# Kernel tuning notes

Measured on AMD Instinct MI355X. Metric: run time of the kernel, lower is better.

The kernel has to match this reference:

```python
import jax, jax.numpy as jnp
import numpy as np

B, L, TOPK, NUM_RBF, NUM_POS, MAX_REL, CH = 4, 1024, 30, 16, 16, 32, 128
EDGE_IN = NUM_POS + NUM_RBF * 25 + 18  # 434
NODE_IN = 22


def _normalize(x, axis=-1):
    n = jnp.linalg.norm(x, axis=axis, keepdims=True)
    return jnp.where(n > 0, x / jnp.where(n > 0, n, 1.0), 0.0)


def layer_norm(x, g, b, eps=1e-5):
    mu = jnp.mean(x, axis=-1, keepdims=True)
    var = jnp.var(x, axis=-1, keepdims=True)
    return (x - mu) / jnp.sqrt(var + eps) * g + b


def gather_nodes_d(nodes, idx):
    # nodes [B,M,C], idx [B,N,K] -> [B,N,K,C]
    Bn, N, K = idx.shape
    out = jnp.take_along_axis(nodes, idx.reshape(Bn, N * K, 1), axis=1)
    return out.reshape(Bn, N, K, nodes.shape[-1])


def gather_edges(edges, idx):
    # edges [B,N,N,C], idx [B,N,K] -> [B,N,K,C]
    return jnp.take_along_axis(edges, idx[..., None], axis=2)


def cal_dihedral(Xf, eps=1e-7):
    U = _normalize(Xf[:, 1:, :] - Xf[:, :-1, :])
    u_0, u_1, u_2 = U[:, :-2], U[:, 1:-1], U[:, 2:]
    n_0 = _normalize(jnp.cross(u_0, u_1))
    n_1 = _normalize(jnp.cross(u_1, u_2))
    cosD = jnp.clip(jnp.sum(n_0 * n_1, -1), -1 + eps, 1 - eps)
    v = _normalize(jnp.cross(n_0, n_1))
    return jnp.sign(jnp.sum(-v * u_1, -1)) * jnp.arccos(cosD)


def _dihedrals(X, eps=1e-7):
    Bn, N = X.shape[0], X.shape[1]
    Xf = X[:, :, :3, :].reshape(Bn, 3 * N, 3)
    D = jnp.pad(cal_dihedral(Xf), ((0, 0), (1, 2))).reshape(Bn, N, 3)
    dihedral_feats = jnp.concatenate([jnp.cos(D), jnp.sin(D)], -1)
    U = _normalize(Xf[:, 1:, :] - Xf[:, :-1, :])
    cosA = jnp.clip(jnp.sum(U[:, :-2] * U[:, 1:-1], -1), -1 + eps, 1 - eps)
    A = jnp.pad(jnp.arccos(cosA), ((0, 0), (1, 2))).reshape(Bn, N, 3)
    angle_feats = jnp.concatenate([jnp.cos(A), jnp.sin(A)], -1)
    return jnp.concatenate([dihedral_feats, angle_feats], -1)  # [B,N,12]


def _quaternions(R):
    diag = jnp.diagonal(R, axis1=-2, axis2=-1)
    Rxx, Ryy, Rzz = diag[..., 0], diag[..., 1], diag[..., 2]
    mags = 0.5 * jnp.sqrt(jnp.abs(1.0 + jnp.stack([Rxx - Ryy - Rzz, -Rxx + Ryy - Rzz, -Rxx - Ryy + Rzz], -1)))
    signs = jnp.sign(jnp.stack([R[..., 2, 1] - R[..., 1, 2], R[..., 0, 2] - R[..., 2, 0], R[..., 1, 0] - R[..., 0, 1]], -1))
    w = jnp.sqrt(jax.nn.relu(1.0 + jnp.sum(diag, -1, keepdims=True))) / 2.0
    return _normalize(jnp.concatenate([signs * mags, w], -1))


def _orientations_coarse_gl_tuple(X, E_idx):
    V = X  # [B,N,4,3]
    Bn, N = X.shape[0], X.shape[1]
    Xf = X[:, :, :3, :].reshape(Bn, 3 * N, 3)
    U = _normalize(Xf[:, 1:, :] - Xf[:, :-1, :])
    u_0, u_1 = U[:, :-2], U[:, 1:-1]
    n_0 = _normalize(jnp.cross(u_0, u_1))[:, ::3]  # [B,N-1,3]
    b_1 = _normalize(u_0 - u_1)[:, ::3]
    Xa = Xf[:, ::3]  # N-atom coords [B,N,3]
    Q = jnp.stack([b_1, n_0, jnp.cross(b_1, n_0)], 2).reshape(Bn, N - 1, 9)
    Q = jnp.pad(Q, ((0, 0), (0, 1), (0, 0)))  # [B,N,9]
    Qm = Q.reshape(Bn, N, 3, 3)
    Q_neighbors = gather_nodes_d(Q, E_idx).reshape(Bn, N, -1, 3, 3)
    X_nb = gather_nodes_d(V[:, :, 1, :], E_idx)
    N_nb = gather_nodes_d(V[:, :, 0, :], E_idx)
    C_nb = gather_nodes_d(V[:, :, 2, :], E_idx)
    O_nb = gather_nodes_d(V[:, :, 3, :], E_idx)
    dXn = jnp.stack([X_nb, N_nb, C_nb, O_nb], 3) - Xa[:, :, None, None, :]  # [B,N,K,4,3]
    dU = jnp.einsum('bnij,bnkaj->bnkai', Qm, dXn)
    Kn = E_idx.shape[-1]
    E_direct = _normalize(dU).reshape(Bn, N, Kn, 12)
    R = jnp.einsum('bnji,bnkjl->bnkil', Qm, Q_neighbors)
    q = _quaternions(R)  # [B,N,K,4]
    dX_inner = V[:, :, jnp.array([0, 2, 3]), :] - Xa[:, :, None, :]
    V_direct = _normalize(jnp.einsum('bnij,bnaj->bnai', Qm, dX_inner)).reshape(Bn, N, 9)
    return V_direct, E_direct, q


def _dist(Xc, mask, eps=1e-6):
    mask_2D = mask[:, None, :] * mask[:, :, None]
    D = mask_2D * jnp.sqrt(jnp.sum((Xc[:, None, :, :] - Xc[:, :, None, :]) ** 2, -1) + eps)
    D_max = jnp.max(D, -1, keepdims=True)
    D_adjust = D + (1.0 - mask_2D) * D_max
    negD, E_idx = jax.lax.top_k(-D_adjust, min(TOPK, Xc.shape[1]))
    return -negD, E_idx


def _dist_seq(res_idx):
    D = jnp.abs(res_idx[:, :, None] - res_idx[:, None, :])
    _, E_idx = jax.lax.top_k(-D, min(TOPK, res_idx.shape[1]))
    return E_idx


def _rbf(D):
    D_mu = jnp.linspace(2.0, 22.0, NUM_RBF)
    D_sigma = (22.0 - 2.0) / NUM_RBF
    return jnp.exp(-(((D[..., None] - D_mu) / D_sigma) ** 2))


def _get_rbf(A, Bm, E_idx):
    D = jnp.sqrt(jnp.sum((A[:, :, None, :] - Bm[:, None, :, :]) ** 2, -1) + 1e-6)
    return _rbf(gather_edges(D[..., None], E_idx)[..., 0])


PAIRS = [('N', 'N'), ('C', 'C'), ('O', 'O'), ('Cb', 'Cb'), ('Ca', 'N'), ('Ca', 'C'), ('Ca', 'O'), ('Ca', 'Cb'),
         ('N', 'C'), ('N', 'O'), ('N', 'Cb'), ('Cb', 'C'), ('Cb', 'O'), ('O', 'C'), ('N', 'Ca'), ('C', 'Ca'),
         ('O', 'Ca'), ('Cb', 'Ca'), ('C', 'N'), ('O', 'N'), ('Cb', 'N'), ('C', 'Cb'), ('O', 'Cb'), ('C', 'O')]


def _forward(X, mask, residue_idx, chain_labels, W_pos, b_pos, W_edge, W_node, g_edge, b_edge, g_node, b_node):
    bvec = X[:, :, 1, :] - X[:, :, 0, :]
    cvec = X[:, :, 2, :] - X[:, :, 1, :]
    avec = jnp.cross(bvec, cvec)
    Cb = -0.58273431 * avec + 0.56802827 * bvec - 0.54067466 * cvec + X[:, :, 1, :]
    atoms = {'N': X[:, :, 0, :], 'Ca': X[:, :, 1, :], 'C': X[:, :, 2, :], 'O': X[:, :, 3, :], 'Cb': Cb}
    D_neighbors, E_idx = _dist(atoms['Ca'], mask)
    E_idx_res = _dist_seq(residue_idx)
    E_idx = jnp.where(mask[:, :, None] == 0, E_idx_res, E_idx)
    RBF_all = [_rbf(D_neighbors)]
    for pa, pb in PAIRS:
        RBF_all.append(_get_rbf(atoms[pa], atoms[pb], E_idx))
    RBF_all = jnp.concatenate(RBF_all, -1)  # [B,L,K,400]
    V_angles = _dihedrals(X) * mask[..., None]
    V_direct, E_direct, E_angles = _orientations_coarse_gl_tuple(X, E_idx)
    V_direct = V_direct * mask[..., None]
    offset = residue_idx[:, :, None] - residue_idx[:, None, :]
    E_offset = gather_edges(offset[..., None], E_idx)[..., 0]
    d_chains = (chain_labels[:, :, None] == chain_labels[:, None, :]).astype(jnp.int32)
    E_chains = gather_edges(d_chains[..., None], E_idx)[..., 0]
    d = jnp.clip(E_offset + MAX_REL, 0, 2 * MAX_REL) * E_chains + (1 - E_chains) * (2 * MAX_REL + 1)
    E_positional = jax.nn.one_hot(d, 2 * MAX_REL + 2, dtype=W_pos.dtype) @ W_pos + b_pos
    mask_j = gather_nodes_d(mask[..., None], E_idx)[..., 0]
    fdt = E_direct.dtype
    E = jnp.concatenate([E_positional, RBF_all, E_direct, E_angles,
                         E_chains[..., None].astype(fdt), mask_j[..., None]], -1)  # [B,L,K,434]
    E = layer_norm(E @ W_edge, g_edge, b_edge)
    Vn = jnp.concatenate([V_angles, V_direct, mask[..., None]], -1)  # [B,L,22]
    Vn = layer_norm(Vn @ W_node, g_node, b_node)
    return Vn, E, E_idx


def setup_inputs():
    key = jax.random.key(0)
    ks = jax.random.split(key, 8)
    X = 3.0 * jax.random.normal(ks[0], (B, L, 4, 3), jnp.float32)
    mask = jnp.ones((B, L), jnp.float32)
    residue_idx = jnp.tile(jnp.arange(L, dtype=jnp.int32), (B, 1))
    chain_labels = jax.random.randint(ks[1], (B, L), 0, 2, dtype=jnp.int32)
    s = lambda k, sh: jax.random.normal(k, sh, jnp.float32) * 0.05
    W_pos = s(ks[2], (2 * MAX_REL + 2, NUM_POS))
    b_pos = jnp.zeros((NUM_POS,), jnp.float32)
    W_edge = s(ks[3], (EDGE_IN, CH))
    W_node = s(ks[4], (NODE_IN, CH))
    return dict(X=X, mask=mask, residue_idx=residue_idx, chain_labels=chain_labels,
                W_pos=W_pos, b_pos=b_pos, W_edge=W_edge, W_node=W_node,
                g_edge=jnp.ones((CH,), jnp.float32), b_edge=jnp.zeros((CH,), jnp.float32),
                g_node=jnp.ones((CH,), jnp.float32), b_node=jnp.zeros((CH,), jnp.float32))


def reference(X, mask, residue_idx, chain_labels, W_pos, b_pos, W_edge, W_node, g_edge, b_edge, g_node, b_node):
    return _forward(X, mask, residue_idx, chain_labels, W_pos, b_pos, W_edge, W_node,
                    g_edge, b_edge, g_node, b_node)
```

## Files before the change

kernel.cpp:

```cpp
#include <hip/hip_runtime.h>

#define BATCH 4
#define LEN   1024
#define KNB   30
#define CH    128
#define EIN   434
#define KP    448
#define KST   14
#define ASTR  456
#define CSTR  132
#define AJS   20

typedef unsigned short ushort_t;
typedef __attribute__((ext_vector_type(8))) short bf16x8;
typedef __attribute__((ext_vector_type(4))) float f32x4;

__constant__ int c_pa[24] = {0,2,3,4,1,1,1,1,0,0,0,4,4,3,0,2,3,4,2,3,4,2,3,2};
__constant__ int c_pb[24] = {0,2,3,4,0,2,3,4,2,3,4,2,3,2,1,1,1,1,0,0,0,4,4,3};

struct F3 { float x, y, z; };
__device__ __forceinline__ F3 f3sub(F3 a, F3 b){ return {a.x-b.x, a.y-b.y, a.z-b.z}; }
__device__ __forceinline__ F3 f3cross(F3 a, F3 b){
  return {a.y*b.z - a.z*b.y, a.z*b.x - a.x*b.z, a.x*b.y - a.y*b.x};
}
__device__ __forceinline__ float f3dot(F3 a, F3 b){ return a.x*b.x + a.y*b.y + a.z*b.z; }
__device__ __forceinline__ F3 f3norm(F3 a){
  float s2 = f3dot(a,a);
  float inv = (s2 > 0.f) ? __builtin_amdgcn_rsqf(s2) : 0.f;
  return {a.x*inv, a.y*inv, a.z*inv};
}
__device__ __forceinline__ float fsign(float x){ return (x > 0.f) ? 1.f : ((x < 0.f) ? -1.f : 0.f); }
__device__ __forceinline__ float clip1(float c){ return fminf(fmaxf(c, -1.f + 1e-7f), 1.f - 1e-7f); }

__device__ __forceinline__ void dihedral_cs(F3 ua, F3 ub, F3 uc, float& c, float& s){
  F3 n0 = f3norm(f3cross(ua, ub));
  F3 n1 = f3norm(f3cross(ub, uc));
  float cd = clip1(f3dot(n0, n1));
  F3 v = f3norm(f3cross(n0, n1));
  c = cd;
  s = fsign(-f3dot(v, ub)) * sqrtf(1.f - cd*cd);
}

__device__ __forceinline__ ushort_t f2bf(float f){
  unsigned u = __float_as_uint(f);
  unsigned r = u + 0x7FFFu + ((u >> 16) & 1u);
  return (ushort_t)(r >> 16);
}

__device__ __forceinline__ unsigned cvt_pk(float a, float b){
  unsigned r;
  asm("v_cvt_pk_bf16_f32 %0, %1, %2" : "=v"(r) : "v"(a), "v"(b));
  return r;
}

__device__ __forceinline__ int corig(int c){
  if (c < 16 || c >= 416) return c;
  int base = (c < 216) ? 16 : 216;
  int p = (c - base) >> 3, m = (c - base) & 7;
  return 16 + p*16 + m + ((c < 216) ? 0 : 8);
}

#define DPP_MIN_STEP(v, ctrl) do{                                            \
    unsigned t_ = (unsigned)__builtin_amdgcn_update_dpp(                     \
        (int)0xFFFFFFFF, (int)(v), (ctrl), 0xF, 0xF, false);                 \
    (v) = t_ < (v) ? t_ : (v);                                               \
  } while(0)
__device__ __forceinline__ unsigned wave_min_u32(unsigned v){
  DPP_MIN_STEP(v, 0x111);
  DPP_MIN_STEP(v, 0x112);
  DPP_MIN_STEP(v, 0x114);
  DPP_MIN_STEP(v, 0x118);
  DPP_MIN_STEP(v, 0x142);
  DPP_MIN_STEP(v, 0x143);
  return (unsigned)__builtin_amdgcn_readlane((int)v, 63);
}

__global__ __launch_bounds__(256) void prep_kernel(
    const float* __restrict__ X, const float* __restrict__ mask,
    const float* __restrict__ We,
    float* __restrict__ wCb, float* __restrict__ wQ, float* __restrict__ wVn,
    float* __restrict__ wCa, ushort_t* __restrict__ Wfrag)
{
  if (blockIdx.x >= 16){
    int f = (blockIdx.x - 16)*256 + threadIdx.x;
    if (f >= 8*KST*64) return;
    int t = f / (KST*64);
    int s = (f / 64) % KST;
    int l = f & 63;
    int n  = t*16 + (l & 15);
    int k0 = s*32 + (l >> 4)*8;
    ushort_t v[8];
    #pragma unroll
    for (int j = 0; j < 8; ++j){
      int k = k0 + j;
      v[j] = (k < EIN) ? f2bf(We[(size_t)corig(k)*CH + n]) : (ushort_t)0;
    }
    ulong2* dst = (ulong2*)(Wfrag + (size_t)f*8);
    *dst = *(ulong2*)v;
    return;
  }

  int idx = blockIdx.x * 256 + threadIdx.x;
  int n = idx & (LEN - 1);
  const float* p = X + (size_t)idx * 12;
  const float4* p4 = (const float4*)p;
  float4 q0 = p4[0], q1 = p4[1], q2 = p4[2];
  F3 Na = {q0.x, q0.y, q0.z};
  F3 Ca = {q0.w, q1.x, q1.y};
  F3 Cc = {q1.z, q1.w, q2.x};
  F3 Oa = {q2.y, q2.z, q2.w};
  ((float4*)wCa)[idx] = make_float4(Ca.x, Ca.y, Ca.z, 0.f);
  F3 bv = f3sub(Ca, Na);
  F3 cv = f3sub(Cc, Ca);
  F3 av = f3cross(bv, cv);
  ((float4*)wCb)[idx] = make_float4(
    -0.58273431f*av.x + 0.56802827f*bv.x - 0.54067466f*cv.x + Ca.x,
    -0.58273431f*av.y + 0.56802827f*bv.y - 0.54067466f*cv.y + Ca.y,
    -0.58273431f*av.z + 0.56802827f*bv.z - 0.54067466f*cv.z + Ca.z, 0.f);

  F3 u0 = f3norm(bv);
  F3 u1 = f3norm(cv);

  float Q[9];
  if (n < LEN - 1){
    F3 b1 = f3norm(f3sub(u0, u1));
    F3 n0 = f3norm(f3cross(u0, u1));
    F3 r2 = f3cross(b1, n0);
    Q[0]=b1.x; Q[1]=b1.y; Q[2]=b1.z;
    Q[3]=n0.x; Q[4]=n0.y; Q[5]=n0.z;
    Q[6]=r2.x; Q[7]=r2.y; Q[8]=r2.z;
  } else {
    #pragma unroll
    for (int t = 0; t < 9; ++t) Q[t] = 0.f;
  }
  float4* wq4 = (float4*)(wQ + (size_t)idx*12);
  wq4[0] = make_float4(Q[0], Q[1], Q[2], Q[3]);
  wq4[1] = make_float4(Q[4], Q[5], Q[6], Q[7]);
  wq4[2] = make_float4(Q[8], 0.f, 0.f, 0.f);

  float m = mask[idx];
  bool hp = (n > 0), hn = (n < LEN - 1);
  F3 um1 = {0,0,0}, u2 = {0,0,0}, u3 = {0,0,0};
  if (hp){
    const float* pp = p - 12;
    F3 Cp = {pp[6], pp[7], pp[8]};
    um1 = f3norm(f3sub(Na, Cp));
  }
  if (hn){
    const float* pn = p + 12;
    F3 Nn  = {pn[0], pn[1], pn[2]};
    F3 Can = {pn[3], pn[4], pn[5]};
    u2 = f3norm(f3sub(Nn, Cc));
    u3 = f3norm(f3sub(Can, Nn));
  }
  float cD0=1.f,sD0=0.f, cD1=1.f,sD1=0.f, cD2=1.f,sD2=0.f;
  float cA0=1.f,sA0=0.f, cA1=1.f,sA1=0.f, cA2=1.f,sA2=0.f;
  if (hp){
    dihedral_cs(um1, u0, u1, cD0, sD0);
    cA0 = clip1(f3dot(um1, u0)); sA0 = sqrtf(1.f - cA0*cA0);
  }
  if (hn){
    dihedral_cs(u0, u1, u2, cD1, sD1);
    dihedral_cs(u1, u2, u3, cD2, sD2);
    cA1 = clip1(f3dot(u0, u1)); sA1 = sqrtf(1.f - cA1*cA1);
    cA2 = clip1(f3dot(u1, u2)); sA2 = sqrtf(1.f - cA2*cA2);
  }
  float vn[22];
  vn[0] = cD0*m; vn[1] = cD1*m; vn[2]  = cD2*m;
  vn[3] = sD0*m; vn[4] = sD1*m; vn[5]  = sD2*m;
  vn[6] = cA0*m; vn[7] = cA1*m; vn[8]  = cA2*m;
  vn[9] = sA0*m; vn[10]= sA1*m; vn[11] = sA2*m;
  F3 dxs[3];
  dxs[0] = {0.f, 0.f, 0.f};
  dxs[1] = f3sub(Cc, Na);
  dxs[2] = f3sub(Oa, Na);
  #pragma unroll
  for (int a = 0; a < 3; ++a){
    F3 dv = dxs[a];
    F3 du = { Q[0]*dv.x + Q[1]*dv.y + Q[2]*dv.z,
              Q[3]*dv.x + Q[4]*dv.y + Q[5]*dv.z,
              Q[6]*dv.x + Q[7]*dv.y + Q[8]*dv.z };
    F3 dn = f3norm(du);
    vn[12 + a*3 + 0] = dn.x * m;
    vn[12 + a*3 + 1] = dn.y * m;
    vn[12 + a*3 + 2] = dn.z * m;
  }
  vn[21] = m;
  #pragma unroll
  for (int t = 0; t < 22; ++t) wVn[(size_t)idx*22 + t] = vn[t];
}

__global__ __launch_bounds__(256) void topk_kernel(
    const float* __restrict__ wCa, const float* __restrict__ wVn,
    const float* __restrict__ Wn,  const float* __restrict__ gn,
    const float* __restrict__ bn,
    float* __restrict__ wDn, int* __restrict__ wIdx,
    float* __restrict__ outI, float* __restrict__ outV)
{
  int wid = threadIdx.x >> 6, l = threadIdx.x & 63;
  int bi = blockIdx.x*4 + wid;
  int b  = bi >> 10;
  const float4* Ca = (const float4*)wCa;
  float4 ci = Ca[bi];
  const float4* Cb = Ca + (size_t)b * LEN;

  unsigned D[16];
  #pragma unroll
  for (int t = 0; t < 16; ++t){
    int j = l + 64*t;
    float4 cj = Cb[j];
    float dx = ci.x - cj.x, dy = ci.y - cj.y, dz = ci.z - cj.z;
    D[t] = __float_as_uint(sqrtf(dx*dx + dy*dy + dz*dz + 1e-6f));
  }
  unsigned lmin = D[0]; unsigned jmin = (unsigned)l;
  #pragma unroll
  for (int t = 1; t < 16; ++t)
    if (D[t] < lmin){ lmin = D[t]; jmin = (unsigned)(l + 64*t); }

  for (int k = 0; k < KNB; ++k){
    unsigned dmin = wave_min_u32(lmin);
    unsigned long long tie = __ballot(lmin == dmin);
    bool iwin;
    unsigned jw;
    if (__popcll(tie) == 1ull){
      iwin = (lmin == dmin);
      jw = jmin;
    } else {
      unsigned cand = (lmin == dmin) ? jmin : 0xFFFFFFFFu;
      jw = wave_min_u32(cand);
      iwin = (cand == jw);
    }
    if (iwin){
      wIdx[bi*KNB + k] = (int)jw;
      wDn[bi*KNB + k]  = __uint_as_float(dmin);
      outI[bi*KNB + k] = (float)jw;
      int tw = (int)(jw >> 6);
      #pragma unroll
      for (int t = 0; t < 16; ++t) if (t == tw) D[t] = 0xFFFFFFFFu;
      lmin = D[0]; jmin = (unsigned)l;
      #pragma unroll
      for (int t = 1; t < 16; ++t)
        if (D[t] < lmin){ lmin = D[t]; jmin = (unsigned)(l + 64*t); }
    }
  }

  float x0 = 0.f, x1 = 0.f;
  #pragma unroll
  for (int r = 0; r < 22; ++r){
    float vr = wVn[(size_t)bi*22 + r];
    x0 = fmaf(vr, Wn[r*CH + l],      x0);
    x1 = fmaf(vr, Wn[r*CH + l + 64], x1);
  }
  float sum = x0 + x1;
  #pragma unroll
  for (int off = 1; off < 64; off <<= 1) sum += __shfl_xor(sum, off);
  float mu = sum * (1.f/128.f);
  float d0 = x0 - mu, d1 = x1 - mu;
  float vs = d0*d0 + d1*d1;
  #pragma unroll
  for (int off = 1; off < 64; off <<= 1) vs += __shfl_xor(vs, off);
  float inv = 1.f / sqrtf(vs * (1.f/128.f) + 1e-5f);
  outV[(size_t)bi*CH + l]      = d0*inv*gn[l]    + bn[l];
  outV[(size_t)bi*CH + l + 64] = d1*inv*gn[l+64] + bn[l+64];
}

__global__ __launch_bounds__(512) void edge_kernel(
    const float* __restrict__ X, const float* __restrict__ mask,
    const int* __restrict__ resi, const int* __restrict__ chain,
    const float* __restrict__ Wp, const float* __restrict__ bp,
    const float* __restrict__ ge, const float* __restrict__ be,
    const float* __restrict__ wCb, const float* __restrict__ wQ,
    const float* __restrict__ wDn, const int* __restrict__ wIdx,
    const ushort_t* __restrict__ Wfrag,
    float* __restrict__ outE)
{
  __shared__ __align__(16) ushort_t As[32*ASTR];
  __shared__ __align__(16) float sAJ[KNB][AJS];
  __shared__ __align__(16) float sAI[16];
  __shared__ __align__(16) float sQi[12];

  int bi  = blockIdx.x;
  int b   = bi >> 10;
  int tid = threadIdx.x;
  int w   = tid >> 6, l = tid & 63;

  float qj0=0.f,qj1=0.f,qj2=0.f,qj3=0.f,qj4=0.f,qj5=0.f,qj6=0.f,qj7=0.f,qj8=0.f;
  if (w == 0 && l < KNB){
    int j  = wIdx[bi*KNB + l];
    int gj = (b << 10) + j;
    const float4* pj4 = (const float4*)(X + (size_t)gj * 12);
    *(float4*)&sAJ[l][0] = pj4[0];
    *(float4*)&sAJ[l][4] = pj4[1];
    *(float4*)&sAJ[l][8] = pj4[2];
  } else if (w == 1 && l < KNB){
    int j  = wIdx[bi*KNB + l];
    int gj = (b << 10) + j;
    *(float4*)&sAJ[l][12] = ((const float4*)wCb)[gj];
    sAJ[l][15] = wDn[bi*KNB + l];
    sAJ[l][16] = (chain[bi] == chain[gj]) ? 1.f : 0.f;
    sAJ[l][17] = mask[gj];
    sAJ[l][18] = (float)(resi[bi] - resi[gj]);
  } else if (w == 2 && l < KNB){
    int j  = wIdx[bi*KNB + l];
    int gj = (b << 10) + j;
    const float4* q4 = (const float4*)(wQ + (size_t)gj * 12);
    float4 a = q4[0], bq = q4[1], cq = q4[2];
    qj0=a.x; qj1=a.y; qj2=a.z; qj3=a.w;
    qj4=bq.x; qj5=bq.y; qj6=bq.z; qj7=bq.w;
    qj8=cq.x;
  } else if (w == 3 && l == 0){
    const float4* pi4 = (const float4*)(X + (size_t)bi * 12);
    *(float4*)&sAI[0]  = pi4[0];
    *(float4*)&sAI[4]  = pi4[1];
    *(float4*)&sAI[8]  = pi4[2];
    *(float4*)&sAI[12] = ((const float4*)wCb)[bi];
  } else if (w == 3 && l == 1){
    const float4* q4 = (const float4*)(wQ + (size_t)bi * 12);
    *(float4*)&sQi[0] = q4[0];
    *(float4*)&sQi[4] = q4[1];
    *(float4*)&sQi[8] = q4[2];
  }
  for (int e = tid; e < KNB*14; e += 512){
    int r = e / 14, c = EIN + (e % 14);
    As[r*ASTR + c] = 0;
  }
  __syncthreads();

  auto rbf_task = [&](int tau){
    int k = (int)(((unsigned)tau * 5243u) >> 17);
    int p = tau - k*25;
    float d;
    if (p == 0) d = sAJ[k][15];
    else {
      int ai = c_pa[p-1]*3, bj = c_pb[p-1]*3;
      float dx = sAI[ai+0] - sAJ[k][bj+0];
      float dy = sAI[ai+1] - sAJ[k][bj+1];
      float dz = sAI[ai+2] - sAJ[k][bj+2];
      d = sqrtf(dx*dx + dy*dy + dz*dz + 1e-6f);
    }
    float A  = d*d*(-0.92332483f);
    float Bc = d*1.84664966f;
    unsigned u[8];
    #pragma unroll
    for (int h = 0; h < 8; ++h){
      float mu0 = 2.f + (2*h  )*(4.f/3.f);
      float mu1 = 2.f + (2*h+1)*(4.f/3.f);
      float e0 = __builtin_amdgcn_exp2f(fmaf(Bc, mu0, A + (-0.92332483f*mu0*mu0)));
      float e1 = __builtin_amdgcn_exp2f(fmaf(Bc, mu1, A + (-0.92332483f*mu1*mu1)));
      u[h] = cvt_pk(e0, e1);
    }
    *(uint4*)&As[k*ASTR + 16  + p*8] = make_uint4(u[0], u[1], u[2], u[3]);
    *(uint4*)&As[k*ASTR + 216 + p*8] = make_uint4(u[4], u[5], u[6], u[7]);
  };

  rbf_task(tid);
  if (tid >= 274) rbf_task(tid + 238);

  if (w == 1 && l < KNB){
    int k = l;
    ushort_t* row = &As[k*ASTR];
    float ch = sAJ[k][16];
    int off  = (int)sAJ[k][18];
    int dpos = off + 32;
    dpos = dpos < 0 ? 0 : (dpos > 64 ? 64 : dpos);
    if (!(ch > 0.5f)) dpos = 65;
    const float4* wp4 = (const float4*)(Wp + dpos*16);
    const float4* bp4 = (const float4*)bp;
    unsigned u[8];
    #pragma unroll
    for (int h = 0; h < 4; ++h){
      float4 wv = wp4[h], bv = bp4[h];
      u[2*h]   = cvt_pk(wv.x + bv.x, wv.y + bv.y);
      u[2*h+1] = cvt_pk(wv.z + bv.z, wv.w + bv.w);
    }
    *(uint4*)&row[0] = make_uint4(u[0], u[1], u[2], u[3]);
    *(uint4*)&row[8] = make_uint4(u[4], u[5], u[6], u[7]);
    *(unsigned*)&row[432] = cvt_pk(ch, sAJ[k][17]);
  } else if (w == 2 && l < KNB){
    int k = l;
    ushort_t* row = &As[k*ASTR];
    float R[3][3];
    R[0][0] = sQi[0]*qj0 + sQi[3]*qj3 + sQi[6]*qj6;
    R[0][1] = sQi[0]*qj1 + sQi[3]*qj4 + sQi[6]*qj7;
    R[0][2] = sQi[0]*qj2 + sQi[3]*qj5 + sQi[6]*qj8;
    R[1][0] = sQi[1]*qj0 + sQi[4]*qj3 + sQi[7]*qj6;
    R[1][1] = sQi[1]*qj1 + sQi[4]*qj4 + sQi[7]*qj7;
    R[1][2] = sQi[1]*qj2 + sQi[4]*qj5 + sQi[7]*qj8;
    R[2][0] = sQi[2]*qj0 + sQi[5]*qj3 + sQi[8]*qj6;
    R[2][1] = sQi[2]*qj1 + sQi[5]*qj4 + sQi[8]*qj7;
    R[2][2] = sQi[2]*qj2 + sQi[5]*qj5 + sQi[8]*qj8;
    float Rxx = R[0][0], Ryy = R[1][1], Rzz = R[2][2];
    float mx = 0.5f*sqrtf(fabsf(1.f + Rxx - Ryy - Rzz));
    float my = 0.5f*sqrtf(fabsf(1.f - Rxx + Ryy - Rzz));
    float mz = 0.5f*sqrtf(fabsf(1.f - Rxx - Ryy + Rzz));
    float qx = fsign(R[2][1] - R[1][2]) * mx;
    float qy = fsign(R[0][2] - R[2][0]) * my;
    float qz = fsign(R[1][0] - R[0][1]) * mz;
    float qw = sqrtf(fmaxf(1.f + Rxx + Ryy + Rzz, 0.f)) * 0.5f;
    float qn2 = qx*qx + qy*qy + qz*qz + qw*qw;
    float inv = qn2 > 0.f ? __builtin_amdgcn_rsqf(qn2) : 0.f;
    *(uint2*)&row[428] = make_uint2(cvt_pk(qx*inv, qy*inv), cvt_pk(qz*inv, qw*inv));
  } else if (w == 3 && l < KNB){
    int k = l;
    ushort_t* row = &As[k*ASTR];
    float nx = sAI[0], ny = sAI[1], nz = sAI[2];
    const int amap[4] = {3, 0, 6, 9};
    float f[12];
    #pragma unroll
    for (int a = 0; a < 4; ++a){
      float dx = sAJ[k][amap[a]+0] - nx;
      float dy = sAJ[k][amap[a]+1] - ny;
      float dz = sAJ[k][amap[a]+2] - nz;
      float e0 = sQi[0]*dx + sQi[1]*dy + sQi[2]*dz;
      float e1 = sQi[3]*dx + sQi[4]*dy + sQi[5]*dz;
      float e2 = sQi[6]*dx + sQi[7]*dy + sQi[8]*dz;
      float ss = e0*e0 + e1*e1 + e2*e2;
      float inv = ss > 0.f ? __builtin_amdgcn_rsqf(ss) : 0.f;
      f[a*3+0] = e0*inv; f[a*3+1] = e1*inv; f[a*3+2] = e2*inv;
    }
    unsigned u[6];
    #pragma unroll
    for (int h = 0; h < 6; ++h) u[h] = cvt_pk(f[2*h], f[2*h+1]);
    *(uint4*)&row[416] = make_uint4(u[0], u[1], u[2], u[3]);
    *(uint2*)&row[424] = make_uint2(u[4], u[5]);
  }
  __syncthreads();

  int aOff0 = (l & 15)*ASTR + (l >> 4)*8;
  int aOff1 = aOff0 + 16*ASTR;
  const ushort_t* bpw = Wfrag + ((size_t)(w*KST)*64 + l)*8;

  f32x4 acc0 = {0.f,0.f,0.f,0.f}, acc1 = acc0;

  bf16x8 a0 = *(const bf16x8*)&As[aOff0];
  bf16x8 a1 = *(const bf16x8*)&As[aOff1];
  bf16x8 b0 = *(const bf16x8*)bpw;
  #pragma unroll
  for (int s = 0; s < KST; ++s){
    bf16x8 a0n, a1n, b0n;
    if (s < KST-1){
      int ka = (s+1)*32;
      a0n = *(const bf16x8*)&As[aOff0 + ka];
      a1n = *(const bf16x8*)&As[aOff1 + ka];
      b0n = *(const bf16x8*)(bpw + (size_t)(s+1)*64*8);
    }
    acc0 = __builtin_amdgcn_mfma_f32_16x16x32_bf16(a0, b0, acc0, 0, 0, 0);
    acc1 = __builtin_amdgcn_mfma_f32_16x16x32_bf16(a1, b0, acc1, 0, 0, 0);
    if (s < KST-1){ a0 = a0n; a1 = a1n; b0 = b0n; }
  }
  __syncthreads();

  float* Cs = (float*)As;
  int ccol = l & 15, crow = (l >> 4)*4;
  #pragma unroll
  for (int r = 0; r < 4; ++r){
    Cs[(crow + r)*CSTR      + w*16 + ccol] = acc0[r];
    Cs[(16 + crow + r)*CSTR + w*16 + ccol] = acc1[r];
  }
  __syncthreads();

  if (tid < KNB*16){
    int row = tid >> 4, g = tid & 15;
    const float4* vr = (const float4*)&Cs[row*CSTR + g*8];
    float4 v0 = vr[0], v1 = vr[1];
    float v[8] = {v0.x,v0.y,v0.z,v0.w, v1.x,v1.y,v1.z,v1.w};
    float s = 0.f;
    #pragma unroll
    for (int c = 0; c < 8; ++c) s += v[c];
    #pragma unroll
    for (int off = 1; off < 16; off <<= 1) s += __shfl_xor(s, off, 16);
    float mu = s * (1.f/128.f);
    float vs = 0.f;
    #pragma unroll
    for (int c = 0; c < 8; ++c){ float dd = v[c] - mu; vs += dd*dd; }
    #pragma unroll
    for (int off = 1; off < 16; off <<= 1) vs += __shfl_xor(vs, off, 16);
    float inv = 1.f / sqrtf(vs * (1.f/128.f) + 1e-5f);
    const float4* g4 = (const float4*)&ge[g*8];
    const float4* b4 = (const float4*)&be[g*8];
    float4 ga = g4[0], gb = g4[1], ba = b4[0], bb = b4[1];
    float4 o0, o1;
    o0.x = (v[0]-mu)*inv*ga.x + ba.x;  o0.y = (v[1]-mu)*inv*ga.y + ba.y;
    o0.z = (v[2]-mu)*inv*ga.z + ba.z;  o0.w = (v[3]-mu)*inv*ga.w + ba.w;
    o1.x = (v[4]-mu)*inv*gb.x + bb.x;  o1.y = (v[5]-mu)*inv*gb.y + bb.y;
    o1.z = (v[6]-mu)*inv*gb.z + bb.z;  o1.w = (v[7]-mu)*inv*gb.w + bb.w;
    float4* dst = (float4*)&outE[((size_t)bi*KNB + row)*CH + g*8];
    dst[0] = o0;
    dst[1] = o1;
  }
}

extern "C" void kernel_launch(void* const* d_in, const int* in_sizes, int n_in,
                              void* d_out, int out_size, void* d_ws, size_t ws_size,
                              hipStream_t stream)
{
  const float* X    = (const float*)d_in[0];
  const float* mask = (const float*)d_in[1];
  const int*   resi = (const int*)  d_in[2];
  const int*   chn  = (const int*)  d_in[3];
  const float* Wp   = (const float*)d_in[4];
  const float* bp   = (const float*)d_in[5];
  const float* We   = (const float*)d_in[6];
  const float* Wn   = (const float*)d_in[7];
  const float* ge   = (const float*)d_in[8];
  const float* be   = (const float*)d_in[9];
  const float* gn   = (const float*)d_in[10];
  const float* bn   = (const float*)d_in[11];

  float* outV = (float*)d_out;
  float* outE = outV + (size_t)BATCH*LEN*CH;
  float* outI = outE + (size_t)BATCH*LEN*KNB*CH;

  float* ws   = (float*)d_ws;
  float* wCb  = ws;
  float* wQ   = wCb + (size_t)BATCH*LEN*4;
  float* wVn  = wQ  + (size_t)BATCH*LEN*12;
  float* wDn  = wVn + (size_t)BATCH*LEN*22;
  int*   wIdx = (int*)(wDn + (size_t)BATCH*LEN*KNB);
  float* wCa  = (float*)(wIdx + (size_t)BATCH*LEN*KNB);
  ushort_t* Wfrag = (ushort_t*)(wCa + (size_t)BATCH*LEN*4);

  prep_kernel<<<16 + 28, 256, 0, stream>>>(X, mask, We, wCb, wQ, wVn, wCa, Wfrag);
  topk_kernel<<<BATCH*LEN/4, 256, 0, stream>>>(wCa, wVn, Wn, gn, bn,
                                               wDn, wIdx, outI, outV);
  edge_kernel<<<BATCH*LEN, 512, 0, stream>>>(X, mask, resi, chn, Wp, bp, ge, be,
                                             wCb, wQ, wDn, wIdx, Wfrag, outE);
}
```

Measured before the change: 155.6 us.

## Fuse prep and top-k kernels into a single front kernel launch

Merges the prep kernel and the top-k/node-feature kernel into one launch. Top-k blocks now read Ca coordinates straight from X and recompute the node features in registers, so the wCa and wVn intermediates are never written or reread. This removes one kernel launch and its dependency boundary. In exchange each top-k wave recomputes the frame math and loads Ca with strided 12-float accesses instead of packed float4.

```diff
diff --git a/kernel.cpp b/kernel.cpp
--- a/kernel.cpp
+++ b/kernel.cpp
@@ -10,6 +10,7 @@
 #define ASTR  456
 #define CSTR  132
 #define AJS   20
+#define NTB   44
 
 typedef unsigned short ushort_t;
 typedef __attribute__((ext_vector_type(8))) short bf16x8;
@@ -75,12 +76,160 @@
   return (unsigned)__builtin_amdgcn_readlane((int)v, 63);
 }
 
-__global__ __launch_bounds__(256) void prep_kernel(
+__global__ __launch_bounds__(256) void front_kernel(
     const float* __restrict__ X, const float* __restrict__ mask,
-    const float* __restrict__ We,
-    float* __restrict__ wCb, float* __restrict__ wQ, float* __restrict__ wVn,
-    float* __restrict__ wCa, ushort_t* __restrict__ Wfrag)
+    const float* __restrict__ We, const float* __restrict__ Wn,
+    const float* __restrict__ gn, const float* __restrict__ bn,
+    float* __restrict__ wCb, float* __restrict__ wQ,
+    float* __restrict__ wDn, int* __restrict__ wIdx,
+    ushort_t* __restrict__ Wfrag,
+    float* __restrict__ outI, float* __restrict__ outV)
 {
+  if (blockIdx.x >= NTB){
+    int wid = threadIdx.x >> 6, l = threadIdx.x & 63;
+    int bi = (blockIdx.x - NTB)*4 + wid;
+    int b  = bi >> 10;
+    const float* Xb = X + (size_t)b * LEN * 12;
+    float cix = X[(size_t)bi*12 + 3];
+    float ciy = X[(size_t)bi*12 + 4];
+    float ciz = X[(size_t)bi*12 + 5];
+
+    unsigned D[16];
+    #pragma unroll
+    for (int t = 0; t < 16; ++t){
+      int j = l + 64*t;
+      const float* pj = Xb + (size_t)j*12;
+      float cjx = pj[3];
+      float2 cyz = *(const float2*)(pj + 4);
+      float dx = cix - cjx, dy = ciy - cyz.x, dz = ciz - cyz.y;
+      D[t] = __float_as_uint(sqrtf(dx*dx + dy*dy + dz*dz + 1e-6f));
+    }
+    unsigned lmin = D[0]; unsigned jmin = (unsigned)l;
+    #pragma unroll
+    for (int t = 1; t < 16; ++t)
+      if (D[t] < lmin){ lmin = D[t]; jmin = (unsigned)(l + 64*t); }
+
+    for (int k = 0; k < KNB; ++k){
+      unsigned dmin = wave_min_u32(lmin);
+      unsigned long long tie = __ballot(lmin == dmin);
+      bool iwin;
+      unsigned jw;
+      if (__popcll(tie) == 1ull){
+        iwin = (lmin == dmin);
+        jw = jmin;
+      } else {
+        unsigned cand = (lmin == dmin) ? jmin : 0xFFFFFFFFu;
+        jw = wave_min_u32(cand);
+        iwin = (cand == jw);
+      }
+      if (iwin){
+        wIdx[bi*KNB + k] = (int)jw;
+        wDn[bi*KNB + k]  = __uint_as_float(dmin);
+        outI[(size_t)bi*KNB + k] = (float)jw;
+        int tw = (int)(jw >> 6);
+        #pragma unroll
+        for (int t = 0; t < 16; ++t) if (t == tw) D[t] = 0xFFFFFFFFu;
+        lmin = D[0]; jmin = (unsigned)l;
+        #pragma unroll
+        for (int t = 1; t < 16; ++t)
+          if (D[t] < lmin){ lmin = D[t]; jmin = (unsigned)(l + 64*t); }
+      }
+    }
+
+    int n = bi & (LEN - 1);
+    const float* p = X + (size_t)bi * 12;
+    const float4* p4 = (const float4*)p;
+    float4 q0 = p4[0], q1 = p4[1], q2 = p4[2];
+    F3 Na = {q0.x, q0.y, q0.z};
+    F3 Ca = {q0.w, q1.x, q1.y};
+    F3 Cc = {q1.z, q1.w, q2.x};
+    F3 Oa = {q2.y, q2.z, q2.w};
+    F3 bv = f3sub(Ca, Na);
+    F3 cv = f3sub(Cc, Ca);
+    F3 u0 = f3norm(bv);
+    F3 u1 = f3norm(cv);
+    float Q[9];
+    if (n < LEN - 1){
+      F3 b1 = f3norm(f3sub(u0, u1));
+      F3 n0 = f3norm(f3cross(u0, u1));
+      F3 r2 = f3cross(b1, n0);
+      Q[0]=b1.x; Q[1]=b1.y; Q[2]=b1.z;
+      Q[3]=n0.x; Q[4]=n0.y; Q[5]=n0.z;
+      Q[6]=r2.x; Q[7]=r2.y; Q[8]=r2.z;
+    } else {
+      #pragma unroll
+      for (int t = 0; t < 9; ++t) Q[t] = 0.f;
+    }
+    float m = mask[bi];
+    bool hp = (n > 0), hn = (n < LEN - 1);
+    F3 um1 = {0,0,0}, u2 = {0,0,0}, u3 = {0,0,0};
+    if (hp){
+      const float* pp = p - 12;
+      F3 Cp = {pp[6], pp[7], pp[8]};
+      um1 = f3norm(f3sub(Na, Cp));
+    }
+    if (hn){
+      const float* pn = p + 12;
+      F3 Nn  = {pn[0], pn[1], pn[2]};
+      F3 Can = {pn[3], pn[4], pn[5]};
+      u2 = f3norm(f3sub(Nn, Cc));
+      u3 = f3norm(f3sub(Can, Nn));
+    }
+    float cD0=1.f,sD0=0.f, cD1=1.f,sD1=0.f, cD2=1.f,sD2=0.f;
+    float cA0=1.f,sA0=0.f, cA1=1.f,sA1=0.f, cA2=1.f,sA2=0.f;
+    if (hp){
+      dihedral_cs(um1, u0, u1, cD0, sD0);
+      cA0 = clip1(f3dot(um1, u0)); sA0 = sqrtf(1.f - cA0*cA0);
+    }
+    if (hn){
+      dihedral_cs(u0, u1, u2, cD1, sD1);
+      dihedral_cs(u1, u2, u3, cD2, sD2);
+      cA1 = clip1(f3dot(u0, u1)); sA1 = sqrtf(1.f - cA1*cA1);
+      cA2 = clip1(f3dot(u1, u2)); sA2 = sqrtf(1.f - cA2*cA2);
+    }
+    float vn[22];
+    vn[0] = cD0*m; vn[1] = cD1*m; vn[2]  = cD2*m;
+    vn[3] = sD0*m; vn[4] = sD1*m; vn[5]  = sD2*m;
+    vn[6] = cA0*m; vn[7] = cA1*m; vn[8]  = cA2*m;
+    vn[9] = sA0*m; vn[10]= sA1*m; vn[11] = sA2*m;
+    F3 dxs[3];
+    dxs[0] = {0.f, 0.f, 0.f};
+    dxs[1] = f3sub(Cc, Na);
+    dxs[2] = f3sub(Oa, Na);
+    #pragma unroll
+    for (int a = 0; a < 3; ++a){
+      F3 dv = dxs[a];
+      F3 du = { Q[0]*dv.x + Q[1]*dv.y + Q[2]*dv.z,
+                Q[3]*dv.x + Q[4]*dv.y + Q[5]*dv.z,
+                Q[6]*dv.x + Q[7]*dv.y + Q[8]*dv.z };
+      F3 dn = f3norm(du);
+      vn[12 + a*3 + 0] = dn.x * m;
+      vn[12 + a*3 + 1] = dn.y * m;
+      vn[12 + a*3 + 2] = dn.z * m;
+    }
+    vn[21] = m;
+
+    float x0 = 0.f, x1 = 0.f;
+    #pragma unroll
+    for (int r = 0; r < 22; ++r){
+      float vr = vn[r];
+      x0 = fmaf(vr, Wn[r*CH + l],      x0);
+      x1 = fmaf(vr, Wn[r*CH + l + 64], x1);
+    }
+    float sum = x0 + x1;
+    #pragma unroll
+    for (int off = 1; off < 64; off <<= 1) sum += __shfl_xor(sum, off);
+    float mu = sum * (1.f/128.f);
+    float d0 = x0 - mu, d1 = x1 - mu;
+    float vs = d0*d0 + d1*d1;
+    #pragma unroll
+    for (int off = 1; off < 64; off <<= 1) vs += __shfl_xor(vs, off);
+    float inv = 1.f / sqrtf(vs * (1.f/128.f) + 1e-5f);
+    outV[(size_t)bi*CH + l]      = d0*inv*gn[l]    + bn[l];
+    outV[(size_t)bi*CH + l + 64] = d1*inv*gn[l+64] + bn[l+64];
+    return;
+  }
+
   if (blockIdx.x >= 16){
     int f = (blockIdx.x - 16)*256 + threadIdx.x;
     if (f >= 8*KST*64) return;
@@ -108,8 +257,6 @@
   F3 Na = {q0.x, q0.y, q0.z};
   F3 Ca = {q0.w, q1.x, q1.y};
   F3 Cc = {q1.z, q1.w, q2.x};
-  F3 Oa = {q2.y, q2.z, q2.w};
-  ((float4*)wCa)[idx] = make_float4(Ca.x, Ca.y, Ca.z, 0.f);
   F3 bv = f3sub(Ca, Na);
   F3 cv = f3sub(Cc, Ca);
   F3 av = f3cross(bv, cv);
@@ -120,7 +267,6 @@
 
   F3 u0 = f3norm(bv);
   F3 u1 = f3norm(cv);
-
   float Q[9];
   if (n < LEN - 1){
     F3 b1 = f3norm(f3sub(u0, u1));
@@ -137,131 +283,6 @@
   wq4[0] = make_float4(Q[0], Q[1], Q[2], Q[3]);
   wq4[1] = make_float4(Q[4], Q[5], Q[6], Q[7]);
   wq4[2] = make_float4(Q[8], 0.f, 0.f, 0.f);
-
-  float m = mask[idx];
-  bool hp = (n > 0), hn = (n < LEN - 1);
-  F3 um1 = {0,0,0}, u2 = {0,0,0}, u3 = {0,0,0};
-  if (hp){
-    const float* pp = p - 12;
-    F3 Cp = {pp[6], pp[7], pp[8]};
-    um1 = f3norm(f3sub(Na, Cp));
-  }
-  if (hn){
-    const float* pn = p + 12;
-    F3 Nn  = {pn[0], pn[1], pn[2]};
-    F3 Can = {pn[3], pn[4], pn[5]};
-    u2 = f3norm(f3sub(Nn, Cc));
-    u3 = f3norm(f3sub(Can, Nn));
-  }
-  float cD0=1.f,sD0=0.f, cD1=1.f,sD1=0.f, cD2=1.f,sD2=0.f;
-  float cA0=1.f,sA0=0.f, cA1=1.f,sA1=0.f, cA2=1.f,sA2=0.f;
-  if (hp){
-    dihedral_cs(um1, u0, u1, cD0, sD0);
-    cA0 = clip1(f3dot(um1, u0)); sA0 = sqrtf(1.f - cA0*cA0);
-  }
-  if (hn){
-    dihedral_cs(u0, u1, u2, cD1, sD1);
-    dihedral_cs(u1, u2, u3, cD2, sD2);
-    cA1 = clip1(f3dot(u0, u1)); sA1 = sqrtf(1.f - cA1*cA1);
-    cA2 = clip1(f3dot(u1, u2)); sA2 = sqrtf(1.f - cA2*cA2);
-  }
-  float vn[22];
-  vn[0] = cD0*m; vn[1] = cD1*m; vn[2]  = cD2*m;
-  vn[3] = sD0*m; vn[4] = sD1*m; vn[5]  = sD2*m;
-  vn[6] = cA0*m; vn[7] = cA1*m; vn[8]  = cA2*m;
-  vn[9] = sA0*m; vn[10]= sA1*m; vn[11] = sA2*m;
-  F3 dxs[3];
-  dxs[0] = {0.f, 0.f, 0.f};
-  dxs[1] = f3sub(Cc, Na);
-  dxs[2] = f3sub(Oa, Na);
-  #pragma unroll
-  for (int a = 0; a < 3; ++a){
-    F3 dv = dxs[a];
-    F3 du = { Q[0]*dv.x + Q[1]*dv.y + Q[2]*dv.z,
-              Q[3]*dv.x + Q[4]*dv.y + Q[5]*dv.z,
-              Q[6]*dv.x + Q[7]*dv.y + Q[8]*dv.z };
-    F3 dn = f3norm(du);
-    vn[12 + a*3 + 0] = dn.x * m;
-    vn[12 + a*3 + 1] = dn.y * m;
-    vn[12 + a*3 + 2] = dn.z * m;
-  }
-  vn[21] = m;
-  #pragma unroll
-  for (int t = 0; t < 22; ++t) wVn[(size_t)idx*22 + t] = vn[t];
-}
-
-__global__ __launch_bounds__(256) void topk_kernel(
-    const float* __restrict__ wCa, const float* __restrict__ wVn,
-    const float* __restrict__ Wn,  const float* __restrict__ gn,
-    const float* __restrict__ bn,
-    float* __restrict__ wDn, int* __restrict__ wIdx,
-    float* __restrict__ outI, float* __restrict__ outV)
-{
-  int wid = threadIdx.x >> 6, l = threadIdx.x & 63;
-  int bi = blockIdx.x*4 + wid;
-  int b  = bi >> 10;
-  const float4* Ca = (const float4*)wCa;
-  float4 ci = Ca[bi];
-  const float4* Cb = Ca + (size_t)b * LEN;
-
-  unsigned D[16];
-  #pragma unroll
-  for (int t = 0; t < 16; ++t){
-    int j = l + 64*t;
-    float4 cj = Cb[j];
-    float dx = ci.x - cj.x, dy = ci.y - cj.y, dz = ci.z - cj.z;
-    D[t] = __float_as_uint(sqrtf(dx*dx + dy*dy + dz*dz + 1e-6f));
-  }
-  unsigned lmin = D[0]; unsigned jmin = (unsigned)l;
-  #pragma unroll
-  for (int t = 1; t < 16; ++t)
-    if (D[t] < lmin){ lmin = D[t]; jmin = (unsigned)(l + 64*t); }
-
-  for (int k = 0; k < KNB; ++k){
-    unsigned dmin = wave_min_u32(lmin);
-    unsigned long long tie = __ballot(lmin == dmin);
-    bool iwin;
-    unsigned jw;
-    if (__popcll(tie) == 1ull){
-      iwin = (lmin == dmin);
-      jw = jmin;
-    } else {
-      unsigned cand = (lmin == dmin) ? jmin : 0xFFFFFFFFu;
-      jw = wave_min_u32(cand);
-      iwin = (cand == jw);
-    }
-    if (iwin){
-      wIdx[bi*KNB + k] = (int)jw;
-      wDn[bi*KNB + k]  = __uint_as_float(dmin);
-      outI[bi*KNB + k] = (float)jw;
-      int tw = (int)(jw >> 6);
-      #pragma unroll
-      for (int t = 0; t < 16; ++t) if (t == tw) D[t] = 0xFFFFFFFFu;
-      lmin = D[0]; jmin = (unsigned)l;
-      #pragma unroll
-      for (int t = 1; t < 16; ++t)
-        if (D[t] < lmin){ lmin = D[t]; jmin = (unsigned)(l + 64*t); }
-    }
-  }
-
-  float x0 = 0.f, x1 = 0.f;
-  #pragma unroll
-  for (int r = 0; r < 22; ++r){
-    float vr = wVn[(size_t)bi*22 + r];
-    x0 = fmaf(vr, Wn[r*CH + l],      x0);
-    x1 = fmaf(vr, Wn[r*CH + l + 64], x1);
-  }
-  float sum = x0 + x1;
-  #pragma unroll
-  for (int off = 1; off < 64; off <<= 1) sum += __shfl_xor(sum, off);
-  float mu = sum * (1.f/128.f);
-  float d0 = x0 - mu, d1 = x1 - mu;
-  float vs = d0*d0 + d1*d1;
-  #pragma unroll
-  for (int off = 1; off < 64; off <<= 1) vs += __shfl_xor(vs, off);
-  float inv = 1.f / sqrtf(vs * (1.f/128.f) + 1e-5f);
-  outV[(size_t)bi*CH + l]      = d0*inv*gn[l]    + bn[l];
-  outV[(size_t)bi*CH + l + 64] = d1*inv*gn[l+64] + bn[l+64];
 }
 
 __global__ __launch_bounds__(512) void edge_kernel(
@@ -514,15 +535,12 @@
   float* ws   = (float*)d_ws;
   float* wCb  = ws;
   float* wQ   = wCb + (size_t)BATCH*LEN*4;
-  float* wVn  = wQ  + (size_t)BATCH*LEN*12;
-  float* wDn  = wVn + (size_t)BATCH*LEN*22;
+  float* wDn  = wQ  + (size_t)BATCH*LEN*12;
   int*   wIdx = (int*)(wDn + (size_t)BATCH*LEN*KNB);
-  float* wCa  = (float*)(wIdx + (size_t)BATCH*LEN*KNB);
-  ushort_t* Wfrag = (ushort_t*)(wCa + (size_t)BATCH*LEN*4);
-
-  prep_kernel<<<16 + 28, 256, 0, stream>>>(X, mask, We, wCb, wQ, wVn, wCa, Wfrag);
-  topk_kernel<<<BATCH*LEN/4, 256, 0, stream>>>(wCa, wVn, Wn, gn, bn,
-                                               wDn, wIdx, outI, outV);
+  ushort_t* Wfrag = (ushort_t*)(wIdx + (size_t)BATCH*LEN*KNB);
+
+  front_kernel<<<NTB + BATCH*LEN/4, 256, 0, stream>>>(
+      X, mask, We, Wn, gn, bn, wCb, wQ, wDn, wIdx, Wfrag, outI, outV);
   edge_kernel<<<BATCH*LEN, 512, 0, stream>>>(X, mask, resi, chn, Wp, bp, ge, be,
                                              wCb, wQ, wDn, wIdx, Wfrag, outE);
 }
```

After: 155.0 us. About the same (-0.4%).
